# Performance work log

Hardware: AMD Instinct MI355X
Metric: run time of the kernel (lower is better)

Reference implementation:

```python
import jax, jax.numpy as jnp
import numpy as np

C = 256
NH = 4  # attention heads
G = 8   # groupnorm groups
EPS = 1e-5


def group_norm(x, weight, bias):
    B, Cc, H, W = x.shape
    xg = x.reshape(B, G, Cc // G, H, W)
    mean = xg.mean(axis=(2, 3, 4), keepdims=True)
    var = xg.var(axis=(2, 3, 4), keepdims=True)
    xg = (xg - mean) * jax.lax.rsqrt(var + EPS)
    xn = xg.reshape(B, Cc, H, W)
    return xn * weight[None, :, None, None] + bias[None, :, None, None]


def setup_inputs() -> dict:
    key = jax.random.key(0)
    ks = jax.random.split(key, 7)
    B, H, W = 16, 32, 32
    x = jax.random.normal(ks[0], (B, C, H, W), dtype=jnp.float32)
    n_weight = jnp.ones((C,), dtype=jnp.float32)
    n_bias = jnp.zeros((C,), dtype=jnp.float32)
    qkv_w = jax.random.normal(ks[1], (3 * C, C), dtype=jnp.float32) * (C ** -0.5)
    qkv_b = jnp.zeros((3 * C,), dtype=jnp.float32)
    p_w = jax.random.normal(ks[2], (C, C), dtype=jnp.float32) * (C ** -0.5)
    p_b = jnp.zeros((C,), dtype=jnp.float32)
    return {"x": x, "n_weight": n_weight, "n_bias": n_bias,
            "qkv_w": qkv_w, "qkv_b": qkv_b, "p_w": p_w, "p_b": p_b}


def reference(x, n_weight, n_bias, qkv_w, qkv_b, p_w, p_b):
    B, Cc, H, W = x.shape
    N = H * W
    dh = Cc // NH
    sc = dh ** -0.5
    xn = group_norm(x, n_weight, n_bias)  # [B,C,H,W]
    xn_flat = xn.reshape(B, Cc, N)
    # 1x1 conv == channel matmul
    qkv = jnp.einsum('oc,bcn->bon', qkv_w, xn_flat) + qkv_b[None, :, None]
    qkv = qkv.reshape(B, 3, NH, dh, N)
    q, k, v = qkv[:, 0], qkv[:, 1], qkv[:, 2]  # [B,h,dh,N]
    a = jax.nn.softmax(jnp.einsum('bhci,bhcj->bhij', q, k) * sc, axis=-1)
    o = jnp.einsum('bhij,bhcj->bhci', a, v).reshape(B, Cc, N)
    proj = jnp.einsum('oc,bcn->bon', p_w, o) + p_b[None, :, None]
    return x + proj.reshape(B, Cc, H, W)
```

## Files before the change

kernel.cpp:

```cpp
#include <hip/hip_runtime.h>
#include <math.h>

typedef unsigned short ushort;
typedef unsigned int uint;
typedef __attribute__((ext_vector_type(8))) short bf16x8;
typedef __attribute__((ext_vector_type(4))) float f32x4;

constexpr int Bc  = 16;
constexpr float EPSc = 1e-5f;
constexpr float QSC  = 0.18033688f;

__device__ inline ushort f2bf(float f) {
    uint u = __float_as_uint(f);
    uint r = (u + 0x7fffu + ((u >> 16) & 1u)) >> 16;
    return (ushort)r;
}
__device__ inline uint pack2(float a, float b) {
    return (uint)f2bf(a) | ((uint)f2bf(b) << 16);
}
__device__ __forceinline__ uint cvt2(float a, float b) {
#if __has_builtin(__builtin_amdgcn_cvt_pk_bf16_f32)
    auto v = __builtin_amdgcn_cvt_pk_bf16_f32(a, b);
    uint u; __builtin_memcpy(&u, &v, 4); return u;
#else
    return pack2(a, b);
#endif
}
#if __has_builtin(__builtin_amdgcn_exp2f)
#define EXP2F(x) __builtin_amdgcn_exp2f(x)
#else
#define EXP2F(x) __expf((x) * 0.69314718f)
#endif
__device__ __forceinline__ void gl_lds16(const ushort* g, ushort* l) {
    __builtin_amdgcn_global_load_lds(
        (const __attribute__((address_space(1))) void*)g,
        (__attribute__((address_space(3))) void*)l, 16, 0, 0);
}

__global__ __launch_bounds__(256) void pre_k(
    const float* __restrict__ x, const float* __restrict__ qkvw,
    const float* __restrict__ pw, float* __restrict__ pstats,
    ushort* __restrict__ wqb, ushort* __restrict__ pwb) {
    int blk = blockIdx.x;
    if (blk < 512) {
        int bg = blk >> 2, part = blk & 3;
        const float4* p = (const float4*)(x + (size_t)bg * 32768 + part * 8192);
        float s = 0.f, s2 = 0.f;
        for (int i = threadIdx.x; i < 2048; i += 256) {
            float4 v = p[i];
            s += v.x + v.y + v.z + v.w;
            s2 += v.x*v.x + v.y*v.y + v.z*v.z + v.w*v.w;
        }
        __shared__ float rs[256], rq[256];
        rs[threadIdx.x] = s; rq[threadIdx.x] = s2;
        __syncthreads();
        for (int off = 128; off > 0; off >>= 1) {
            if (threadIdx.x < (unsigned)off) {
                rs[threadIdx.x] += rs[threadIdx.x + off];
                rq[threadIdx.x] += rq[threadIdx.x + off];
            }
            __syncthreads();
        }
        if (threadIdx.x == 0) {
            pstats[blk * 2]     = rs[0];
            pstats[blk * 2 + 1] = rq[0];
        }
    } else {
        int idx = ((blk - 512) * 256 + threadIdx.x) * 4;
        if (idx < 196608) {
            int row = idx >> 8;
            float sc = (row < 256) ? QSC : 1.f;
            float4 v = *(const float4*)&qkvw[idx];
            uint2 u; u.x = pack2(v.x * sc, v.y * sc); u.y = pack2(v.z * sc, v.w * sc);
            *(uint2*)&wqb[idx] = u;
        } else {
            int j = idx - 196608;
            float4 v = *(const float4*)&pw[j];
            uint2 u; u.x = pack2(v.x, v.y); u.y = pack2(v.z, v.w);
            *(uint2*)&pwb[j] = u;
        }
    }
}

__global__ __launch_bounds__(256) void norm_t_k(
    const float* __restrict__ x, const float* __restrict__ pstats,
    const float* __restrict__ nw, const float* __restrict__ nb,
    ushort* __restrict__ xt) {
    int b = blockIdx.z, ct = blockIdx.y, nt = blockIdx.x;
    __shared__ ushort T[64 * 72];
    int t = threadIdx.x;
    int nn4 = (t & 15) * 4;
#pragma unroll
    for (int p = 0; p < 4; ++p) {
        int cl = (t >> 4) + p * 16;
        int c = ct * 64 + cl;
        int g = c >> 5;
        int base = (b * 8 + g) * 8;
        float s  = (pstats[base] + pstats[base+2]) + (pstats[base+4] + pstats[base+6]);
        float s2 = (pstats[base+1] + pstats[base+3]) + (pstats[base+5] + pstats[base+7]);
        float inv_n = 1.f / 32768.f;
        float mean = s * inv_n;
        float var  = s2 * inv_n - mean * mean;
        float inv  = rsqrtf(var + EPSc);
        float sw = inv * nw[c];
        float sb = nb[c] - mean * sw;
        float4 v = *(const float4*)&x[((size_t)(b * 256 + c)) * 1024 + nt * 64 + nn4];
        T[(nn4 + 0) * 72 + cl] = f2bf(v.x * sw + sb);
        T[(nn4 + 1) * 72 + cl] = f2bf(v.y * sw + sb);
        T[(nn4 + 2) * 72 + cl] = f2bf(v.z * sw + sb);
        T[(nn4 + 3) * 72 + cl] = f2bf(v.w * sw + sb);
    }
    __syncthreads();
#pragma unroll
    for (int p = 0; p < 4; ++p) {
        int nn = (t >> 4) + p * 16;
        int c4 = (t & 15) * 4;
        uint2 w = *(const uint2*)&T[nn * 72 + c4];
        *(uint2*)&xt[((size_t)b * 1024 + nt * 64 + nn) * 256 + ct * 64 + c4] = w;
    }
}

__global__ __launch_bounds__(256, 2) void qkv_gemm_k(
    const ushort* __restrict__ wq, const ushort* __restrict__ xt,
    const float* __restrict__ wb, ushort* __restrict__ qkT,
    ushort* __restrict__ vbuf) {
    int b = blockIdx.z, cy = blockIdx.y, sx = blockIdx.x;
    __shared__ ushort SB[2][2][128 * 64];
    int t = threadIdx.x, lane = t & 63, w = t >> 6;
    int quad = lane >> 4, l15 = lane & 15;
    int wm = w >> 1, wn = w & 1;
    const ushort* wrow = wq + (size_t)cy * 128 * 256;
    const ushort* xrow = xt + ((size_t)b * 1024 + sx * 128) * 256;
    bool tpath = (cy < 4);
    int r0 = t >> 3;
    int cs = (t & 7) ^ (r0 & 7);
    int dst = t * 8;
#pragma unroll
    for (int ps = 0; ps < 4; ++ps) {
        int r = r0 + ps * 32;
        gl_lds16(&wrow[(size_t)r * 256 + cs * 8], &SB[0][0][ps * 2048 + dst]);
        gl_lds16(&xrow[(size_t)r * 256 + cs * 8], &SB[0][1][ps * 2048 + dst]);
    }
    __syncthreads();
    int s0 = quad ^ (l15 & 7);
    f32x4 acc[4][4] = {};
    int cur = 0;
    for (int ki = 0; ki < 4; ++ki) {
        if (ki < 3) {
            int k0 = (ki + 1) * 64, nx = cur ^ 1;
#pragma unroll
            for (int ps = 0; ps < 4; ++ps) {
                int r = r0 + ps * 32;
                gl_lds16(&wrow[(size_t)r * 256 + k0 + cs * 8], &SB[nx][0][ps * 2048 + dst]);
                gl_lds16(&xrow[(size_t)r * 256 + k0 + cs * 8], &SB[nx][1][ps * 2048 + dst]);
            }
        }
        const ushort* Wc = SB[cur][0];
        const ushort* Xc = SB[cur][1];
        const ushort* Am = tpath ? Xc : Wc;
        const ushort* Bn = tpath ? Wc : Xc;
#pragma unroll
        for (int kk = 0; kk < 2; ++kk) {
            int sl = s0 ^ (kk * 4);
            bf16x8 fa[4], fb[4];
#pragma unroll
            for (int mi = 0; mi < 4; ++mi)
                fa[mi] = *(const bf16x8*)&Am[(wm * 64 + mi * 16 + l15) * 64 + sl * 8];
#pragma unroll
            for (int ni = 0; ni < 4; ++ni)
                fb[ni] = *(const bf16x8*)&Bn[(wn * 64 + ni * 16 + l15) * 64 + sl * 8];
#pragma unroll
            for (int mi = 0; mi < 4; ++mi)
#pragma unroll
                for (int ni = 0; ni < 4; ++ni)
                    acc[mi][ni] = __builtin_amdgcn_mfma_f32_16x16x32_bf16(
                        fa[mi], fb[ni], acc[mi][ni], 0, 0, 0);
        }
        __syncthreads();
        cur ^= 1;
    }
    __syncthreads();
    ushort* Tw = ((ushort*)SB) + w * (64 * 72);
    float bsc = (tpath && cy < 2) ? QSC : 1.f;
    if (tpath) {
#pragma unroll
        for (int ni = 0; ni < 4; ++ni) {
            float bias = wb[cy * 128 + wn * 64 + ni * 16 + l15] * bsc;
#pragma unroll
            for (int mi = 0; mi < 4; ++mi)
#pragma unroll
                for (int rr = 0; rr < 4; ++rr)
                    Tw[(mi * 16 + quad * 4 + rr) * 72 + ni * 16 + l15] =
                        f2bf(acc[mi][ni][rr] + bias);
        }
    } else {
#pragma unroll
        for (int mi = 0; mi < 4; ++mi)
#pragma unroll
            for (int rr = 0; rr < 4; ++rr) {
                float bias = wb[cy * 128 + wm * 64 + mi * 16 + quad * 4 + rr];
#pragma unroll
                for (int ni = 0; ni < 4; ++ni)
                    Tw[(mi * 16 + quad * 4 + rr) * 72 + ni * 16 + l15] =
                        f2bf(acc[mi][ni][rr] + bias);
            }
    }
    __asm__ __volatile__("" ::: "memory");
    int row8 = lane >> 3, ch = lane & 7;
#pragma unroll
    for (int p = 0; p < 8; ++p) {
        int row = p * 8 + row8;
        uint4 u = *(const uint4*)&Tw[row * 72 + ch * 8];
        if (tpath) {
            int sp = sx * 128 + wm * 64 + row;
            *(uint4*)&qkT[((size_t)b * 1024 + sp) * 512 + cy * 128 + wn * 64 + ch * 8] = u;
        } else {
            int chanloc = (cy - 4) * 128 + wm * 64 + row;
            *(uint4*)&vbuf[((size_t)b * 256 + chanloc) * 1024 + sx * 128 + wn * 64 + ch * 8] = u;
        }
    }
}

__global__ __launch_bounds__(256, 3) void attn_k(
    const ushort* __restrict__ qkT, const ushort* __restrict__ vbuf,
    ushort* __restrict__ ot) {
    int bh = blockIdx.x;
    int i0 = blockIdx.y * 128;
    int b = bh >> 2, h = bh & 3;
    const ushort* qTb = qkT + (size_t)b * 1024 * 512 + h * 64;
    const ushort* kTb = qTb + 256;
    const ushort* vb  = vbuf + ((size_t)(b * 256 + h * 64)) * 1024;
    __shared__ ushort Ks[2][4096], Vs[2][4096];
    __shared__ ushort Ps[8 * 1152];
    __shared__ float  Lx[128];
    int t = threadIdx.x, lane = t & 63, w = t >> 6;
    int quad = lane >> 4, l15 = lane & 15;
    bf16x8 aq[2][2];
#pragma unroll
    for (int rb = 0; rb < 2; ++rb) {
        const ushort* qr = &qTb[(size_t)(i0 + rb * 64 + w * 16 + l15) * 512];
        aq[rb][0] = *(const bf16x8*)&qr[quad * 8];
        aq[rb][1] = *(const bf16x8*)&qr[32 + quad * 8];
    }
    int r0 = t >> 3;
    int cs = (t & 7) ^ (r0 & 7);
    int p0 = quad ^ (l15 & 7);
    int p1 = p0 ^ 4;
    gl_lds16(&kTb[(size_t)r0 * 512 + cs * 8],        &Ks[0][t * 8]);
    gl_lds16(&kTb[(size_t)(r0 + 32) * 512 + cs * 8], &Ks[0][t * 8 + 2048]);
    gl_lds16(&vb[(size_t)r0 * 1024 + cs * 8],        &Vs[0][t * 8]);
    gl_lds16(&vb[(size_t)(r0 + 32) * 1024 + cs * 8], &Vs[0][t * 8 + 2048]);
    __syncthreads();
    float lsum0 = 0.f, lsum1 = 0.f;
    f32x4 oacc[2][4] = {};
    ushort* Pw0 = &Ps[(w * 2 + 0) * 1152];
    ushort* Pw1 = &Ps[(w * 2 + 1) * 1152];
    int cur = 0;
    for (int j0 = 0; j0 < 1024; j0 += 64) {
        if (j0 < 960) {
            int jn = j0 + 64, nx = cur ^ 1;
            gl_lds16(&kTb[(size_t)(jn + r0) * 512 + cs * 8],        &Ks[nx][t * 8]);
            gl_lds16(&kTb[(size_t)(jn + r0 + 32) * 512 + cs * 8],   &Ks[nx][t * 8 + 2048]);
            gl_lds16(&vb[(size_t)r0 * 1024 + jn + cs * 8],          &Vs[nx][t * 8]);
            gl_lds16(&vb[(size_t)(r0 + 32) * 1024 + jn + cs * 8],   &Vs[nx][t * 8 + 2048]);
        }
        const ushort* Kc = Ks[cur];
        const ushort* Vc = Vs[cur];
        f32x4 s0[4], s1[4];
#pragma unroll
        for (int jt = 0; jt < 4; ++jt) {
            int row = jt * 16 + l15;
            bf16x8 bk0 = *(const bf16x8*)&Kc[row * 64 + p0 * 8];
            bf16x8 bk1 = *(const bf16x8*)&Kc[row * 64 + p1 * 8];
            f32x4 a = {0.f, 0.f, 0.f, 0.f};
            a = __builtin_amdgcn_mfma_f32_16x16x32_bf16(bk0, aq[0][0], a, 0, 0, 0);
            a = __builtin_amdgcn_mfma_f32_16x16x32_bf16(bk1, aq[0][1], a, 0, 0, 0);
            s0[jt] = a;
            f32x4 c = {0.f, 0.f, 0.f, 0.f};
            c = __builtin_amdgcn_mfma_f32_16x16x32_bf16(bk0, aq[1][0], c, 0, 0, 0);
            c = __builtin_amdgcn_mfma_f32_16x16x32_bf16(bk1, aq[1][1], c, 0, 0, 0);
            s1[jt] = c;
        }
#pragma unroll
        for (int jt = 0; jt < 4; ++jt) {
            int o = l15 * 72 + jt * 16 + quad * 4;
            float e0 = EXP2F(s0[jt][0]), e1 = EXP2F(s0[jt][1]);
            float e2 = EXP2F(s0[jt][2]), e3 = EXP2F(s0[jt][3]);
            lsum0 += (e0 + e1) + (e2 + e3);
            *(uint*)&Pw0[o]     = cvt2(e0, e1);
            *(uint*)&Pw0[o + 2] = cvt2(e2, e3);
            float f0 = EXP2F(s1[jt][0]), f1 = EXP2F(s1[jt][1]);
            float f2 = EXP2F(s1[jt][2]), f3 = EXP2F(s1[jt][3]);
            lsum1 += (f0 + f1) + (f2 + f3);
            *(uint*)&Pw1[o]     = cvt2(f0, f1);
            *(uint*)&Pw1[o + 2] = cvt2(f2, f3);
        }
        __asm__ __volatile__("" ::: "memory");
        bf16x8 ap00 = *(const bf16x8*)&Pw0[l15 * 72 + quad * 8];
        bf16x8 ap01 = *(const bf16x8*)&Pw0[l15 * 72 + 32 + quad * 8];
        bf16x8 ap10 = *(const bf16x8*)&Pw1[l15 * 72 + quad * 8];
        bf16x8 ap11 = *(const bf16x8*)&Pw1[l15 * 72 + 32 + quad * 8];
#pragma unroll
        for (int ct = 0; ct < 4; ++ct) {
            int row = ct * 16 + l15;
            bf16x8 bv0 = *(const bf16x8*)&Vc[row * 64 + p0 * 8];
            bf16x8 bv1 = *(const bf16x8*)&Vc[row * 64 + p1 * 8];
            oacc[0][ct] = __builtin_amdgcn_mfma_f32_16x16x32_bf16(ap00, bv0, oacc[0][ct], 0, 0, 0);
            oacc[0][ct] = __builtin_amdgcn_mfma_f32_16x16x32_bf16(ap01, bv1, oacc[0][ct], 0, 0, 0);
            oacc[1][ct] = __builtin_amdgcn_mfma_f32_16x16x32_bf16(ap10, bv0, oacc[1][ct], 0, 0, 0);
            oacc[1][ct] = __builtin_amdgcn_mfma_f32_16x16x32_bf16(ap11, bv1, oacc[1][ct], 0, 0, 0);
        }
        __syncthreads();
        cur ^= 1;
    }
    lsum0 += __shfl_xor(lsum0, 16); lsum0 += __shfl_xor(lsum0, 32);
    lsum1 += __shfl_xor(lsum1, 16); lsum1 += __shfl_xor(lsum1, 32);
    if (quad == 0) {
        Lx[w * 16 + l15]      = lsum0;
        Lx[64 + w * 16 + l15] = lsum1;
    }
    __asm__ __volatile__("" ::: "memory");
#pragma unroll
    for (int rb = 0; rb < 2; ++rb) {
        float4 lv = *(const float4*)&Lx[rb * 64 + w * 16 + quad * 4];
        float linv[4] = {1.f / lv.x, 1.f / lv.y, 1.f / lv.z, 1.f / lv.w};
        ushort* Pw = (rb == 0) ? Pw0 : Pw1;
#pragma unroll
        for (int ct = 0; ct < 4; ++ct)
#pragma unroll
            for (int rr = 0; rr < 4; ++rr)
                Pw[(quad * 4 + rr) * 72 + ct * 16 + l15] = f2bf(oacc[rb][ct][rr] * linv[rr]);
        __asm__ __volatile__("" ::: "memory");
#pragma unroll
        for (int p = 0; p < 2; ++p) {
            int row = p * 8 + (lane >> 3), ch = lane & 7;
            uint4 u = *(const uint4*)&Pw[row * 72 + ch * 8];
            *(uint4*)&ot[((size_t)b * 1024 + i0 + rb * 64 + w * 16 + row) * 256 + h * 64 + ch * 8] = u;
        }
    }
}

__global__ __launch_bounds__(256, 3) void proj_k(
    const ushort* __restrict__ pwb, const ushort* __restrict__ ot,
    const float* __restrict__ pb, const float* __restrict__ x,
    float* __restrict__ out) {
    int b = blockIdx.z, cy = blockIdx.y, sx = blockIdx.x;
    __shared__ ushort SB[2][12288];
    int t = threadIdx.x, lane = t & 63, w = t >> 6;
    int quad = lane >> 4, l15 = lane & 15;
    int wm = w >> 1, wn = w & 1;
    const ushort* wrow = pwb + (size_t)cy * 128 * 256;
    const ushort* xrow = ot + ((size_t)b * 1024 + sx * 64) * 256;
    int r0 = t >> 3;
    int cs = (t & 7) ^ (r0 & 7);
    int dst = t * 8;
#pragma unroll
    for (int ps = 0; ps < 4; ++ps)
        gl_lds16(&wrow[(size_t)(r0 + ps * 32) * 256 + cs * 8], &SB[0][ps * 2048 + dst]);
#pragma unroll
    for (int ps = 0; ps < 2; ++ps)
        gl_lds16(&xrow[(size_t)(r0 + ps * 32) * 256 + cs * 8], &SB[0][8192 + ps * 2048 + dst]);
    __syncthreads();
    int p0 = quad ^ (l15 & 7);
    f32x4 acc[4][2] = {};
    int cur = 0;
    for (int ki = 0; ki < 4; ++ki) {
        if (ki < 3) {
            int k0 = (ki + 1) * 64, nx = cur ^ 1;
#pragma unroll
            for (int ps = 0; ps < 4; ++ps)
                gl_lds16(&wrow[(size_t)(r0 + ps * 32) * 256 + k0 + cs * 8], &SB[nx][ps * 2048 + dst]);
#pragma unroll
            for (int ps = 0; ps < 2; ++ps)
                gl_lds16(&xrow[(size_t)(r0 + ps * 32) * 256 + k0 + cs * 8], &SB[nx][8192 + ps * 2048 + dst]);
        }
        const ushort* Wc = &SB[cur][0];
        const ushort* Xc = &SB[cur][8192];
#pragma unroll
        for (int kk = 0; kk < 2; ++kk) {
            int sl = p0 ^ (kk * 4);
            bf16x8 fa[4], fb[2];
#pragma unroll
            for (int mi = 0; mi < 4; ++mi)
                fa[mi] = *(const bf16x8*)&Wc[(wm * 64 + mi * 16 + l15) * 64 + sl * 8];
#pragma unroll
            for (int ni = 0; ni < 2; ++ni)
                fb[ni] = *(const bf16x8*)&Xc[(wn * 32 + ni * 16 + l15) * 64 + sl * 8];
#pragma unroll
            for (int mi = 0; mi < 4; ++mi)
#pragma unroll
                for (int ni = 0; ni < 2; ++ni)
                    acc[mi][ni] = __builtin_amdgcn_mfma_f32_16x16x32_bf16(
                        fa[mi], fb[ni], acc[mi][ni], 0, 0, 0);
        }
        __syncthreads();
        cur ^= 1;
    }
#pragma unroll
    for (int mi = 0; mi < 4; ++mi)
#pragma unroll
        for (int rr = 0; rr < 4; ++rr) {
            int chan = cy * 128 + wm * 64 + mi * 16 + quad * 4 + rr;
            float bias = pb[chan];
#pragma unroll
            for (int ni = 0; ni < 2; ++ni) {
                int sp = sx * 64 + wn * 32 + ni * 16 + l15;
                size_t o = ((size_t)(b * 256 + chan)) * 1024 + sp;
                out[o] = acc[mi][ni][rr] + bias + x[o];
            }
        }
}

extern "C" void kernel_launch(void* const* d_in, const int* in_sizes, int n_in,
                              void* d_out, int out_size, void* d_ws, size_t ws_size,
                              hipStream_t stream) {
    const float* x    = (const float*)d_in[0];
    const float* nw   = (const float*)d_in[1];
    const float* nb   = (const float*)d_in[2];
    const float* qkvw = (const float*)d_in[3];
    const float* qkvb = (const float*)d_in[4];
    const float* pw   = (const float*)d_in[5];
    const float* pb   = (const float*)d_in[6];
    float* out = (float*)d_out;

    float* pstats = (float*)d_ws;
    ushort* base = (ushort*)((char*)d_ws + 4096);
    ushort* xt   = base;
    ushort* wqb  = xt + (size_t)16 * 1024 * 256;
    ushort* pwb  = wqb + 768 * 256;
    ushort* qkT  = pwb + 256 * 256;
    ushort* vbuf = qkT + (size_t)16 * 1024 * 512;
    ushort* ot   = xt;

    pre_k<<<dim3(768), dim3(256), 0, stream>>>(x, qkvw, pw, pstats, wqb, pwb);
    norm_t_k<<<dim3(16, 4, Bc), dim3(256), 0, stream>>>(x, pstats, nw, nb, xt);
    qkv_gemm_k<<<dim3(8, 6, Bc), dim3(256), 0, stream>>>(wqb, xt, qkvb, qkT, vbuf);
    attn_k<<<dim3(64, 8), dim3(256), 0, stream>>>(qkT, vbuf, ot);
    proj_k<<<dim3(16, 2, Bc), dim3(256), 0, stream>>>(pwb, ot, pb, x, out);
}
```

Baseline: 132.8 us.

## Compute softmax row sums via MFMA with ones, use hardware bf16 convert, add setprio

Drops the per-element VALU row-sum accumulation and shuffle/LDS reduction in attention. The row sums now come from extra MFMAs that multiply the bf16 probability tiles by a ones vector, which also keeps the numerator and denominator consistent because both use the rounded bf16 values. Software bf16 rounding is replaced with inline-asm v_cvt_pk_bf16_f32 across all kernels, P stores are packed into uint2, and s_setprio hints are placed around the MFMA sections. This adds MFMA work per tile and relies on the inline-asm instruction being available on the target.

```diff
diff --git a/kernel.cpp b/kernel.cpp
--- a/kernel.cpp
+++ b/kernel.cpp
@@ -19,12 +19,14 @@
     return (uint)f2bf(a) | ((uint)f2bf(b) << 16);
 }
 __device__ __forceinline__ uint cvt2(float a, float b) {
-#if __has_builtin(__builtin_amdgcn_cvt_pk_bf16_f32)
-    auto v = __builtin_amdgcn_cvt_pk_bf16_f32(a, b);
-    uint u; __builtin_memcpy(&u, &v, 4); return u;
-#else
-    return pack2(a, b);
-#endif
+    uint r;
+    asm("v_cvt_pk_bf16_f32 %0, %1, %2" : "=v"(r) : "v"(a), "v"(b));
+    return r;
+}
+__device__ __forceinline__ ushort f2bf_fast(float f) {
+    uint r;
+    asm("v_cvt_pk_bf16_f32 %0, %1, %2" : "=v"(r) : "v"(f), "v"(f));
+    return (ushort)r;
 }
 #if __has_builtin(__builtin_amdgcn_exp2f)
 #define EXP2F(x) __builtin_amdgcn_exp2f(x)
@@ -71,12 +73,12 @@
             int row = idx >> 8;
             float sc = (row < 256) ? QSC : 1.f;
             float4 v = *(const float4*)&qkvw[idx];
-            uint2 u; u.x = pack2(v.x * sc, v.y * sc); u.y = pack2(v.z * sc, v.w * sc);
+            uint2 u; u.x = cvt2(v.x * sc, v.y * sc); u.y = cvt2(v.z * sc, v.w * sc);
             *(uint2*)&wqb[idx] = u;
         } else {
             int j = idx - 196608;
             float4 v = *(const float4*)&pw[j];
-            uint2 u; u.x = pack2(v.x, v.y); u.y = pack2(v.z, v.w);
+            uint2 u; u.x = cvt2(v.x, v.y); u.y = cvt2(v.z, v.w);
             *(uint2*)&pwb[j] = u;
         }
     }
@@ -105,10 +107,10 @@
         float sw = inv * nw[c];
         float sb = nb[c] - mean * sw;
         float4 v = *(const float4*)&x[((size_t)(b * 256 + c)) * 1024 + nt * 64 + nn4];
-        T[(nn4 + 0) * 72 + cl] = f2bf(v.x * sw + sb);
-        T[(nn4 + 1) * 72 + cl] = f2bf(v.y * sw + sb);
-        T[(nn4 + 2) * 72 + cl] = f2bf(v.z * sw + sb);
-        T[(nn4 + 3) * 72 + cl] = f2bf(v.w * sw + sb);
+        T[(nn4 + 0) * 72 + cl] = f2bf_fast(v.x * sw + sb);
+        T[(nn4 + 1) * 72 + cl] = f2bf_fast(v.y * sw + sb);
+        T[(nn4 + 2) * 72 + cl] = f2bf_fast(v.z * sw + sb);
+        T[(nn4 + 3) * 72 + cl] = f2bf_fast(v.w * sw + sb);
     }
     __syncthreads();
 #pragma unroll
@@ -191,7 +193,7 @@
 #pragma unroll
                 for (int rr = 0; rr < 4; ++rr)
                     Tw[(mi * 16 + quad * 4 + rr) * 72 + ni * 16 + l15] =
-                        f2bf(acc[mi][ni][rr] + bias);
+                        f2bf_fast(acc[mi][ni][rr] + bias);
         }
     } else {
 #pragma unroll
@@ -202,7 +204,7 @@
 #pragma unroll
                 for (int ni = 0; ni < 4; ++ni)
                     Tw[(mi * 16 + quad * 4 + rr) * 72 + ni * 16 + l15] =
-                        f2bf(acc[mi][ni][rr] + bias);
+                        f2bf_fast(acc[mi][ni][rr] + bias);
             }
     }
     __asm__ __volatile__("" ::: "memory");
@@ -232,7 +234,6 @@
     const ushort* vb  = vbuf + ((size_t)(b * 256 + h * 64)) * 1024;
     __shared__ ushort Ks[2][4096], Vs[2][4096];
     __shared__ ushort Ps[8 * 1152];
-    __shared__ float  Lx[128];
     int t = threadIdx.x, lane = t & 63, w = t >> 6;
     int quad = lane >> 4, l15 = lane & 15;
     bf16x8 aq[2][2];
@@ -242,6 +243,9 @@
         aq[rb][0] = *(const bf16x8*)&qr[quad * 8];
         aq[rb][1] = *(const bf16x8*)&qr[32 + quad * 8];
     }
+    bf16x8 vones;
+#pragma unroll
+    for (int i = 0; i < 8; ++i) vones[i] = (short)0x3F80;
     int r0 = t >> 3;
     int cs = (t & 7) ^ (r0 & 7);
     int p0 = quad ^ (l15 & 7);
@@ -251,8 +255,9 @@
     gl_lds16(&vb[(size_t)r0 * 1024 + cs * 8],        &Vs[0][t * 8]);
     gl_lds16(&vb[(size_t)(r0 + 32) * 1024 + cs * 8], &Vs[0][t * 8 + 2048]);
     __syncthreads();
-    float lsum0 = 0.f, lsum1 = 0.f;
     f32x4 oacc[2][4] = {};
+    f32x4 lacc0 = {0.f, 0.f, 0.f, 0.f};
+    f32x4 lacc1 = {0.f, 0.f, 0.f, 0.f};
     ushort* Pw0 = &Ps[(w * 2 + 0) * 1152];
     ushort* Pw1 = &Ps[(w * 2 + 1) * 1152];
     int cur = 0;
@@ -267,6 +272,7 @@
         const ushort* Kc = Ks[cur];
         const ushort* Vc = Vs[cur];
         f32x4 s0[4], s1[4];
+        __builtin_amdgcn_s_setprio(1);
 #pragma unroll
         for (int jt = 0; jt < 4; ++jt) {
             int row = jt * 16 + l15;
@@ -281,25 +287,29 @@
             c = __builtin_amdgcn_mfma_f32_16x16x32_bf16(bk1, aq[1][1], c, 0, 0, 0);
             s1[jt] = c;
         }
+        __builtin_amdgcn_s_setprio(0);
 #pragma unroll
         for (int jt = 0; jt < 4; ++jt) {
             int o = l15 * 72 + jt * 16 + quad * 4;
             float e0 = EXP2F(s0[jt][0]), e1 = EXP2F(s0[jt][1]);
             float e2 = EXP2F(s0[jt][2]), e3 = EXP2F(s0[jt][3]);
-            lsum0 += (e0 + e1) + (e2 + e3);
-            *(uint*)&Pw0[o]     = cvt2(e0, e1);
-            *(uint*)&Pw0[o + 2] = cvt2(e2, e3);
+            uint2 u0; u0.x = cvt2(e0, e1); u0.y = cvt2(e2, e3);
+            *(uint2*)&Pw0[o] = u0;
             float f0 = EXP2F(s1[jt][0]), f1 = EXP2F(s1[jt][1]);
             float f2 = EXP2F(s1[jt][2]), f3 = EXP2F(s1[jt][3]);
-            lsum1 += (f0 + f1) + (f2 + f3);
-            *(uint*)&Pw1[o]     = cvt2(f0, f1);
-            *(uint*)&Pw1[o + 2] = cvt2(f2, f3);
+            uint2 u1; u1.x = cvt2(f0, f1); u1.y = cvt2(f2, f3);
+            *(uint2*)&Pw1[o] = u1;
         }
         __asm__ __volatile__("" ::: "memory");
         bf16x8 ap00 = *(const bf16x8*)&Pw0[l15 * 72 + quad * 8];
         bf16x8 ap01 = *(const bf16x8*)&Pw0[l15 * 72 + 32 + quad * 8];
         bf16x8 ap10 = *(const bf16x8*)&Pw1[l15 * 72 + quad * 8];
         bf16x8 ap11 = *(const bf16x8*)&Pw1[l15 * 72 + 32 + quad * 8];
+        __builtin_amdgcn_s_setprio(1);
+        lacc0 = __builtin_amdgcn_mfma_f32_16x16x32_bf16(ap00, vones, lacc0, 0, 0, 0);
+        lacc0 = __builtin_amdgcn_mfma_f32_16x16x32_bf16(ap01, vones, lacc0, 0, 0, 0);
+        lacc1 = __builtin_amdgcn_mfma_f32_16x16x32_bf16(ap10, vones, lacc1, 0, 0, 0);
+        lacc1 = __builtin_amdgcn_mfma_f32_16x16x32_bf16(ap11, vones, lacc1, 0, 0, 0);
 #pragma unroll
         for (int ct = 0; ct < 4; ++ct) {
             int row = ct * 16 + l15;
@@ -310,26 +320,20 @@
             oacc[1][ct] = __builtin_amdgcn_mfma_f32_16x16x32_bf16(ap10, bv0, oacc[1][ct], 0, 0, 0);
             oacc[1][ct] = __builtin_amdgcn_mfma_f32_16x16x32_bf16(ap11, bv1, oacc[1][ct], 0, 0, 0);
         }
+        __builtin_amdgcn_s_setprio(0);
         __syncthreads();
         cur ^= 1;
     }
-    lsum0 += __shfl_xor(lsum0, 16); lsum0 += __shfl_xor(lsum0, 32);
-    lsum1 += __shfl_xor(lsum1, 16); lsum1 += __shfl_xor(lsum1, 32);
-    if (quad == 0) {
-        Lx[w * 16 + l15]      = lsum0;
-        Lx[64 + w * 16 + l15] = lsum1;
-    }
-    __asm__ __volatile__("" ::: "memory");
 #pragma unroll
     for (int rb = 0; rb < 2; ++rb) {
-        float4 lv = *(const float4*)&Lx[rb * 64 + w * 16 + quad * 4];
-        float linv[4] = {1.f / lv.x, 1.f / lv.y, 1.f / lv.z, 1.f / lv.w};
+        f32x4 lv = (rb == 0) ? lacc0 : lacc1;
+        float linv[4] = {1.f / lv[0], 1.f / lv[1], 1.f / lv[2], 1.f / lv[3]};
         ushort* Pw = (rb == 0) ? Pw0 : Pw1;
 #pragma unroll
         for (int ct = 0; ct < 4; ++ct)
 #pragma unroll
             for (int rr = 0; rr < 4; ++rr)
-                Pw[(quad * 4 + rr) * 72 + ct * 16 + l15] = f2bf(oacc[rb][ct][rr] * linv[rr]);
+                Pw[(quad * 4 + rr) * 72 + ct * 16 + l15] = f2bf_fast(oacc[rb][ct][rr] * linv[rr]);
         __asm__ __volatile__("" ::: "memory");
 #pragma unroll
         for (int p = 0; p < 2; ++p) {
```

New measurement: 128.8 us. -3.0%, faster.
